# Optimization experiments

Hardware: AMD Instinct MI355X
Metric: run time of the kernel (lower is better)

Reference implementation:

```python
import jax, jax.numpy as jnp
import numpy as np

B, D, T, K = 16, 512, 4096, 1024
COMMIT = 0.25


def setup_inputs() -> dict:
    key = jax.random.key(0)
    kx, ke = jax.random.split(key)
    x = jax.random.normal(kx, (B, D, T), dtype=jnp.float32)
    # nn.init.uniform_(weight, -1/K, 1/K)
    embedding = jax.random.uniform(ke, (K, D), dtype=jnp.float32,
                                   minval=-1.0 / K, maxval=1.0 / K)
    return {"x": x, "embedding": embedding}


def reference(x, embedding):
    # x: [B, D, T] -> [B, T, D]
    xt = jnp.transpose(x, (0, 2, 1))
    xf = xt.reshape(-1, xt.shape[-1])  # [N, D], N = B*T
    dist = (jnp.sum(xf * xf, axis=1, keepdims=True)
            + jnp.sum(embedding * embedding, axis=1)
            - 2.0 * (xf @ embedding.T))
    idx = jnp.argmin(dist, axis=1)  # [N]
    # one-hot @ embedding == gather
    quantized = jnp.take(embedding, idx, axis=0).reshape(xt.shape)  # [B, T, D]
    commitment_loss = COMMIT * jnp.mean((jax.lax.stop_gradient(quantized) - xt) ** 2)
    embedding_loss = jnp.mean((quantized - jax.lax.stop_gradient(xt)) ** 2)
    loss = commitment_loss + embedding_loss
    # straight-through estimator
    quantized_st = xt + jax.lax.stop_gradient(quantized - xt)
    encoding_indices = idx.reshape(xt.shape[0], xt.shape[1], 1)
    return quantized_st, loss, encoding_indices
```

## Files before the change

### kernel.cpp

```cpp
#include <hip/hip_runtime.h>

#define BB 16
#define DD 512
#define TT 4096
#define KK 1024
#define NN (BB*TT)
#define RWS 64
#define BT 1024
#define NW 16
#define MARGIN 1e-3f
#define CM 6
#define PM 384
#define XLD 516
#define NPART (NN/RWS)

typedef __attribute__((ext_vector_type(8))) short short8v;
typedef __attribute__((ext_vector_type(4))) float f32x4;

__device__ __forceinline__ unsigned short f2bf(float f) {
    unsigned int u = __float_as_uint(f);
    unsigned int r = (u + 0x7fffu + ((u >> 16) & 1u)) >> 16;
    return (unsigned short)r;
}

__device__ __forceinline__ float pw128_sq_strided(const float* a, int stride) {
    float V[16];
    #pragma unroll
    for (int l = 0; l < 16; ++l) {
        float q[8];
        #pragma unroll
        for (int k = 0; k < 8; ++k) {
            float e = a[(l + 16 * k) * stride];
            q[k] = __fmul_rn(e, e);
        }
        V[l] = __fadd_rn(__fadd_rn(__fadd_rn(q[0], q[1]), __fadd_rn(q[2], q[3])),
                         __fadd_rn(__fadd_rn(q[4], q[5]), __fadd_rn(q[6], q[7])));
    }
    float u[8];
    #pragma unroll
    for (int l = 0; l < 8; ++l) u[l] = __fadd_rn(V[l], V[l + 8]);
    float v[4];
    #pragma unroll
    for (int l = 0; l < 4; ++l) v[l] = __fadd_rn(u[l], u[l + 4]);
    return __fadd_rn(__fadd_rn(v[0], v[2]), __fadd_rn(v[1], v[3]));
}
__device__ __forceinline__ float pw512_sq_strided(const float* a, int stride) {
    float p0 = pw128_sq_strided(a, stride);
    float p1 = pw128_sq_strided(a + 128 * stride, stride);
    float p2 = pw128_sq_strided(a + 256 * stride, stride);
    float p3 = pw128_sq_strided(a + 384 * stride, stride);
    return __fadd_rn(__fadd_rn(p0, p1), __fadd_rn(p2, p3));
}

__global__ void enorms_exact(const float* __restrict__ E, float* __restrict__ se) {
    int i = blockIdx.x * blockDim.x + threadIdx.x;
    if (i < KK) se[i] = pw512_sq_strided(E + (long)i * DD, 1);
}

__global__ void pack_e(const float* __restrict__ E, unsigned short* __restrict__ Bph) {
    int i = blockIdx.x * blockDim.x + threadIdx.x;
    if (i >= KK * DD / 2) return;
    int c = i >> 8;
    int k = (i & 255) * 2;
    float2 v = *reinterpret_cast<const float2*>(E + ((long)c << 9) + k);
    int lane = (c & 15) + ((k >> 3) & 3) * 16;
    int hw = (((c >> 4) * 16 + (k >> 5)) * 64 + lane) * 8 + (k & 7);
    unsigned int pk = (unsigned int)f2bf(v.x) | ((unsigned int)f2bf(v.y) << 16);
    *reinterpret_cast<unsigned int*>(Bph + hw) = pk;
}

__device__ __forceinline__ short8v build_frag_rm(const float* __restrict__ row, int c0) {
    union { short8v v; unsigned int wd[4]; } u;
    float4 a = *reinterpret_cast<const float4*>(row + c0);
    float4 b = *reinterpret_cast<const float4*>(row + c0 + 4);
    asm("v_cvt_pk_bf16_f32 %0, %1, %2" : "=v"(u.wd[0]) : "v"(a.x), "v"(a.y));
    asm("v_cvt_pk_bf16_f32 %0, %1, %2" : "=v"(u.wd[1]) : "v"(a.z), "v"(a.w));
    asm("v_cvt_pk_bf16_f32 %0, %1, %2" : "=v"(u.wd[2]) : "v"(b.x), "v"(b.y));
    asm("v_cvt_pk_bf16_f32 %0, %1, %2" : "=v"(u.wd[3]) : "v"(b.z), "v"(b.w));
    return u.v;
}

__global__ __launch_bounds__(BT)
void vq_fused(const float* __restrict__ x, const float* __restrict__ E,
              const unsigned short* __restrict__ Bph,
              const float* __restrict__ se,
              double* __restrict__ partials, float* __restrict__ out) {
    __shared__ __align__(16) float xsf[RWS * XLD];
    __shared__ float wrowmin[NW * RWS];
    __shared__ float gthr[RWS];
    __shared__ int   rcnt[RWS];
    __shared__ unsigned short rc[RWS][CM];
    __shared__ int   prow[PM];
    __shared__ int   pcand[PM];
    __shared__ unsigned long long rmin[RWS];
    __shared__ float sxs[RWS];
    __shared__ int   fidx[RWS];
    __shared__ int   oflag[RWS];
    __shared__ double wloss[NW];
    __shared__ int   pcnt, oany;

    const int tid  = threadIdx.x;
    const int w    = tid >> 6;
    const int lane = tid & 63;
    const int blk  = blockIdx.x;
    const int b    = blk >> 6;
    const int t0   = (blk & 63) * RWS;
    const long nbase = (long)b * TT + t0;
    const float* xb = x + (long)b * DD * TT + t0;

    if (tid < RWS) { rcnt[tid] = 0; rmin[tid] = ~0ull; oflag[tid] = 0; fidx[tid] = -1; }
    if (tid == 0) { pcnt = 0; oany = 0; }

    #pragma unroll
    for (int it = 0; it < 8; ++it) {
        int flat = it * BT + tid;
        int d  = flat >> 4;
        int r4 = (flat & 15) * 4;
        float4 v = *reinterpret_cast<const float4*>(xb + (long)d * TT + r4);
        xsf[(r4 + 0) * XLD + d] = v.x;
        xsf[(r4 + 1) * XLD + d] = v.y;
        xsf[(r4 + 2) * XLD + d] = v.z;
        xsf[(r4 + 3) * XLD + d] = v.w;
    }
    __syncthreads();

    f32x4 acc[4][4];
    #pragma unroll
    for (int m = 0; m < 4; ++m)
        #pragma unroll
        for (int n = 0; n < 4; ++n)
            acc[m][n] = (f32x4){0.f, 0.f, 0.f, 0.f};

    const short8v* Bhv = (const short8v*)Bph;
    {
        const int rl  = lane & 15;
        const int lg8 = (lane >> 4) * 8;
        for (int kk = 0; kk < 16; ++kk) {
            short8v bh[4];
            #pragma unroll
            for (int n = 0; n < 4; ++n)
                bh[n] = Bhv[((w * 4 + n) * 16 + kk) * 64 + lane];
            short8v ah[4];
            #pragma unroll
            for (int m = 0; m < 4; ++m)
                ah[m] = build_frag_rm(xsf + (m * 16 + rl) * XLD, kk * 32 + lg8);
            #pragma unroll
            for (int n = 0; n < 4; ++n)
                #pragma unroll
                for (int m = 0; m < 4; ++m)
                    acc[m][n] = __builtin_amdgcn_mfma_f32_16x16x32_bf16(ah[m], bh[n], acc[m][n], 0, 0, 0);
        }
    }

    float sef[4];
    #pragma unroll
    for (int n = 0; n < 4; ++n) sef[n] = se[w * 64 + n * 16 + (lane & 15)];

    #pragma unroll
    for (int m = 0; m < 4; ++m) {
        #pragma unroll
        for (int r4 = 0; r4 < 4; ++r4) {
            float mn = 1e30f;
            #pragma unroll
            for (int n = 0; n < 4; ++n)
                mn = fminf(mn, fmaf(-2.f, acc[m][n][r4], sef[n]));
            #pragma unroll
            for (int off = 1; off < 16; off <<= 1)
                mn = fminf(mn, __shfl_xor(mn, off, 64));
            if ((lane & 15) == 0)
                wrowmin[w * RWS + m * 16 + (lane >> 4) * 4 + r4] = mn;
        }
    }
    __syncthreads();

    if (tid < RWS) {
        float g = 1e30f;
        #pragma unroll
        for (int ww = 0; ww < NW; ++ww)
            g = fminf(g, wrowmin[ww * RWS + tid]);
        gthr[tid] = g + MARGIN;
    }
    __syncthreads();

    #pragma unroll
    for (int m = 0; m < 4; ++m) {
        #pragma unroll
        for (int r4 = 0; r4 < 4; ++r4) {
            int row = m * 16 + (lane >> 4) * 4 + r4;
            float th = gthr[row];
            #pragma unroll
            for (int n = 0; n < 4; ++n) {
                float sc = fmaf(-2.f, acc[m][n][r4], sef[n]);
                if (sc <= th) {
                    int pos = atomicAdd(&rcnt[row], 1);
                    if (pos < CM)
                        rc[row][pos] = (unsigned short)(w * 64 + n * 16 + (lane & 15));
                }
            }
        }
    }
    {
        int r = tid >> 4, l = tid & 15;
        const float* bp = xsf + r * XLD;
        float pblk[4];
        #pragma unroll
        for (int kb = 0; kb < 4; ++kb) {
            float q[8];
            #pragma unroll
            for (int k = 0; k < 8; ++k) {
                float e = bp[kb * 128 + l + 16 * k];
                q[k] = __fmul_rn(e, e);
            }
            float V = __fadd_rn(__fadd_rn(__fadd_rn(q[0], q[1]), __fadd_rn(q[2], q[3])),
                                __fadd_rn(__fadd_rn(q[4], q[5]), __fadd_rn(q[6], q[7])));
            V = __fadd_rn(V, __shfl_xor(V, 8, 16));
            V = __fadd_rn(V, __shfl_xor(V, 4, 16));
            V = __fadd_rn(V, __shfl_xor(V, 2, 16));
            V = __fadd_rn(V, __shfl_xor(V, 1, 16));
            pblk[kb] = V;
        }
        if (l == 0)
            sxs[r] = __fadd_rn(__fadd_rn(pblk[0], pblk[1]), __fadd_rn(pblk[2], pblk[3]));
    }
    __syncthreads();

    if (tid < RWS) {
        int cnt = rcnt[tid];
        if (cnt == 1) {
            fidx[tid] = (int)rc[tid][0];
        } else if (cnt <= CM) {
            int base = atomicAdd(&pcnt, cnt);
            for (int i = 0; i < cnt; ++i) {
                prow[base + i]  = tid;
                pcand[base + i] = (int)rc[tid][i];
            }
        } else {
            oflag[tid] = 1;
            atomicOr(&oany, 1);
        }
    }
    __syncthreads();

    const int np = (pcnt < PM) ? pcnt : PM;
    {
        int p = lane * NW + w;
        if (p < np) {
            int r = prow[p], c = pcand[p];
            const float4* Ep4 = reinterpret_cast<const float4*>(E + (long)c * DD);
            const float4* Xp4 = reinterpret_cast<const float4*>(xsf + r * XLD);
            float g = 0.f;
            #pragma unroll 4
            for (int jj = 0; jj < 128; ++jj) {
                float4 e4 = Ep4[jj], x4 = Xp4[jj];
                g = __fmaf_rn(x4.x, e4.x, g);
                g = __fmaf_rn(x4.y, e4.y, g);
                g = __fmaf_rn(x4.z, e4.z, g);
                g = __fmaf_rn(x4.w, e4.w, g);
            }
            float t1 = __fadd_rn(sxs[r], se[c]);
            float d  = __fsub_rn(t1, __fmul_rn(2.f, g));
            unsigned int bb = __float_as_uint(d);
            unsigned int u  = (bb & 0x80000000u) ? ~bb : (bb | 0x80000000u);
            atomicMin(&rmin[r], ((unsigned long long)u << 10) | (unsigned int)c);
        }
    }
    __syncthreads();

    if (tid < RWS && fidx[tid] < 0 && !oflag[tid])
        fidx[tid] = (int)(rmin[tid] & 0x3ffu);

    if (oany) {
        for (int r = 0; r < RWS; ++r) {
            if (!oflag[r]) continue;
            const float4* Xp4 = reinterpret_cast<const float4*>(xsf + r * XLD);
            int c = tid;
            const float4* Ep4 = reinterpret_cast<const float4*>(E + (long)c * DD);
            float g = 0.f;
            #pragma unroll 4
            for (int jj = 0; jj < 128; ++jj) {
                float4 e4 = Ep4[jj], x4 = Xp4[jj];
                g = __fmaf_rn(x4.x, e4.x, g);
                g = __fmaf_rn(x4.y, e4.y, g);
                g = __fmaf_rn(x4.z, e4.z, g);
                g = __fmaf_rn(x4.w, e4.w, g);
            }
            float bd = __fsub_rn(__fadd_rn(sxs[r], se[c]), __fmul_rn(2.f, g));
            int bi = c;
            #pragma unroll
            for (int off = 32; off; off >>= 1) {
                float tv = __shfl_down(bd, off, 64);
                int   ti = __shfl_down(bi, off, 64);
                if (tv < bd || (tv == bd && ti < bi)) { bd = tv; bi = ti; }
            }
            if (lane == 0) {
                unsigned int bb = __float_as_uint(bd);
                unsigned int u  = (bb & 0x80000000u) ? ~bb : (bb | 0x80000000u);
                atomicMin(&rmin[r], ((unsigned long long)u << 10) | (unsigned int)bi);
            }
            __syncthreads();
            if (tid == 0) fidx[r] = (int)(rmin[r] & 0x3ffu);
        }
    }
    __syncthreads();

    if (tid < RWS)
        out[(size_t)NN * DD + 1 + nbase + tid] = (float)fidx[tid];

    double lacc = 0.0;
    #pragma unroll
    for (int it = 0; it < 8; ++it) {
        int flat = it * BT + tid;
        int r = flat >> 7;
        int j = (flat & 127) * 4;
        int idx = fidx[r];
        float4 ev = *reinterpret_cast<const float4*>(E + (long)idx * DD + j);
        float4 xv = *reinterpret_cast<const float4*>(&xsf[r * XLD + j]);
        float d0 = __fsub_rn(ev.x, xv.x);
        float d1 = __fsub_rn(ev.y, xv.y);
        float d2 = __fsub_rn(ev.z, xv.z);
        float d3 = __fsub_rn(ev.w, xv.w);
        float4 st;
        st.x = __fadd_rn(xv.x, d0); st.y = __fadd_rn(xv.y, d1);
        st.z = __fadd_rn(xv.z, d2); st.w = __fadd_rn(xv.w, d3);
        *reinterpret_cast<float4*>(out + (size_t)(nbase + r) * DD + j) = st;
        lacc += (double)d0 * d0 + (double)d1 * d1 + (double)d2 * d2 + (double)d3 * d3;
    }
    #pragma unroll
    for (int off = 32; off; off >>= 1) lacc += __shfl_down(lacc, off, 64);
    if (lane == 0) wloss[w] = lacc;
    __syncthreads();
    if (tid == 0) {
        double s = 0.0;
        #pragma unroll
        for (int ww = 0; ww < NW; ++ww) s += wloss[ww];
        partials[blk] = s;
    }
}

__global__ void finalize_kernel(const double* __restrict__ partials, float* __restrict__ out) {
    __shared__ double sm[16];
    const int tid = threadIdx.x;
    const int w = tid >> 6, lane = tid & 63;
    double a = partials[tid];
    #pragma unroll
    for (int off = 32; off; off >>= 1) a += __shfl_down(a, off, 64);
    if (lane == 0) sm[w] = a;
    __syncthreads();
    if (tid == 0) {
        double s = 0.0;
        #pragma unroll
        for (int i = 0; i < 16; ++i) s += sm[i];
        out[(size_t)NN * DD] = (float)(1.25 * s / ((double)NN * DD));
    }
}

extern "C" void kernel_launch(void* const* d_in, const int* in_sizes, int n_in,
                              void* d_out, int out_size, void* d_ws, size_t ws_size,
                              hipStream_t stream) {
    const float* x = (const float*)d_in[0];
    const float* E = (const float*)d_in[1];
    float* out = (float*)d_out;
    double* partials = (double*)d_ws;
    float* se = (float*)((char*)d_ws + 32768);
    unsigned short* Bph = (unsigned short*)((char*)d_ws + 65536);

    enorms_exact<<<4, 256, 0, stream>>>(E, se);
    pack_e<<<(KK * DD / 2) / 256, 256, 0, stream>>>(E, Bph);
    vq_fused<<<NPART, BT, 0, stream>>>(x, E, Bph, se, partials, out);
    finalize_kernel<<<1, 1024, 0, stream>>>(partials, out);
}
```

Before: 258.6 us.

## Halve rows per block, widen per-wave codebook tile, rewrite transposed x load

Each block now handles 32 rows with 8 waves of 512 threads instead of 64 rows with 16 waves, and each wave covers 128 codebook entries with a 2x8 MFMA accumulator tile instead of 4x4. The grid doubles, the finalize kernel sums two partials per thread, and the overflow fallback loops over two codes per thread. The x tile load is rewritten so each lane reads 8 strided d values for one row and writes them as contiguous float4 stores into shared memory. The aim is to shrink shared memory per block for better occupancy and to cut LDS bank conflicts in the transpose, at the cost of loading each B fragment once per 32 rows rather than once per 64.

```diff
diff --git a/kernel.cpp b/kernel.cpp
--- a/kernel.cpp
+++ b/kernel.cpp
@@ -5,12 +5,12 @@
 #define TT 4096
 #define KK 1024
 #define NN (BB*TT)
-#define RWS 64
-#define BT 1024
-#define NW 16
+#define RWS 32
+#define BT 512
+#define NW 8
 #define MARGIN 1e-3f
 #define CM 6
-#define PM 384
+#define PM 192
 #define XLD 516
 #define NPART (NN/RWS)
 
@@ -103,32 +103,38 @@
     const int w    = tid >> 6;
     const int lane = tid & 63;
     const int blk  = blockIdx.x;
-    const int b    = blk >> 6;
-    const int t0   = (blk & 63) * RWS;
+    const int b    = blk >> 7;
+    const int t0   = (blk & 127) * RWS;
     const long nbase = (long)b * TT + t0;
     const float* xb = x + (long)b * DD * TT + t0;
 
     if (tid < RWS) { rcnt[tid] = 0; rmin[tid] = ~0ull; oflag[tid] = 0; fidx[tid] = -1; }
     if (tid == 0) { pcnt = 0; oany = 0; }
 
-    #pragma unroll
-    for (int it = 0; it < 8; ++it) {
-        int flat = it * BT + tid;
-        int d  = flat >> 4;
-        int r4 = (flat & 15) * 4;
-        float4 v = *reinterpret_cast<const float4*>(xb + (long)d * TT + r4);
-        xsf[(r4 + 0) * XLD + d] = v.x;
-        xsf[(r4 + 1) * XLD + d] = v.y;
-        xsf[(r4 + 2) * XLD + d] = v.z;
-        xsf[(r4 + 3) * XLD + d] = v.w;
-    }
-    __syncthreads();
-
-    f32x4 acc[4][4];
-    #pragma unroll
-    for (int m = 0; m < 4; ++m)
-        #pragma unroll
-        for (int n = 0; n < 4; ++n)
+    {
+        const int r  = lane & 31;
+        const int dh = lane >> 5;
+        const float* xbl = xb + r;
+        #pragma unroll
+        for (int it = 0; it < 4; ++it) {
+            int d0 = ((it * NW + w) * 2 + dh) * 8;
+            float v[8];
+            #pragma unroll
+            for (int jj = 0; jj < 8; ++jj)
+                v[jj] = xbl[(long)(d0 + jj) * TT];
+            float4 lo = {v[0], v[1], v[2], v[3]};
+            float4 hi = {v[4], v[5], v[6], v[7]};
+            *reinterpret_cast<float4*>(&xsf[r * XLD + d0])     = lo;
+            *reinterpret_cast<float4*>(&xsf[r * XLD + d0 + 4]) = hi;
+        }
+    }
+    __syncthreads();
+
+    f32x4 acc[2][8];
+    #pragma unroll
+    for (int m = 0; m < 2; ++m)
+        #pragma unroll
+        for (int n = 0; n < 8; ++n)
             acc[m][n] = (f32x4){0.f, 0.f, 0.f, 0.f};
 
     const short8v* Bhv = (const short8v*)Bph;
@@ -136,33 +142,37 @@
         const int rl  = lane & 15;
         const int lg8 = (lane >> 4) * 8;
         for (int kk = 0; kk < 16; ++kk) {
-            short8v bh[4];
-            #pragma unroll
-            for (int n = 0; n < 4; ++n)
-                bh[n] = Bhv[((w * 4 + n) * 16 + kk) * 64 + lane];
-            short8v ah[4];
-            #pragma unroll
-            for (int m = 0; m < 4; ++m)
+            short8v ah[2];
+            #pragma unroll
+            for (int m = 0; m < 2; ++m)
                 ah[m] = build_frag_rm(xsf + (m * 16 + rl) * XLD, kk * 32 + lg8);
             #pragma unroll
-            for (int n = 0; n < 4; ++n)
+            for (int nh = 0; nh < 2; ++nh) {
+                short8v bh[4];
                 #pragma unroll
-                for (int m = 0; m < 4; ++m)
-                    acc[m][n] = __builtin_amdgcn_mfma_f32_16x16x32_bf16(ah[m], bh[n], acc[m][n], 0, 0, 0);
-        }
-    }
-
-    float sef[4];
-    #pragma unroll
-    for (int n = 0; n < 4; ++n) sef[n] = se[w * 64 + n * 16 + (lane & 15)];
-
-    #pragma unroll
-    for (int m = 0; m < 4; ++m) {
+                for (int q = 0; q < 4; ++q)
+                    bh[q] = Bhv[((w * 8 + nh * 4 + q) * 16 + kk) * 64 + lane];
+                #pragma unroll
+                for (int q = 0; q < 4; ++q)
+                    #pragma unroll
+                    for (int m = 0; m < 2; ++m)
+                        acc[m][nh * 4 + q] = __builtin_amdgcn_mfma_f32_16x16x32_bf16(
+                            ah[m], bh[q], acc[m][nh * 4 + q], 0, 0, 0);
+            }
+        }
+    }
+
+    float sef[8];
+    #pragma unroll
+    for (int n = 0; n < 8; ++n) sef[n] = se[w * 128 + n * 16 + (lane & 15)];
+
+    #pragma unroll
+    for (int m = 0; m < 2; ++m) {
         #pragma unroll
         for (int r4 = 0; r4 < 4; ++r4) {
             float mn = 1e30f;
             #pragma unroll
-            for (int n = 0; n < 4; ++n)
+            for (int n = 0; n < 8; ++n)
                 mn = fminf(mn, fmaf(-2.f, acc[m][n][r4], sef[n]));
             #pragma unroll
             for (int off = 1; off < 16; off <<= 1)
@@ -183,18 +193,18 @@
     __syncthreads();
 
     #pragma unroll
-    for (int m = 0; m < 4; ++m) {
+    for (int m = 0; m < 2; ++m) {
         #pragma unroll
         for (int r4 = 0; r4 < 4; ++r4) {
             int row = m * 16 + (lane >> 4) * 4 + r4;
             float th = gthr[row];
             #pragma unroll
-            for (int n = 0; n < 4; ++n) {
+            for (int n = 0; n < 8; ++n) {
                 float sc = fmaf(-2.f, acc[m][n][r4], sef[n]);
                 if (sc <= th) {
                     int pos = atomicAdd(&rcnt[row], 1);
                     if (pos < CM)
-                        rc[row][pos] = (unsigned short)(w * 64 + n * 16 + (lane & 15));
+                        rc[row][pos] = (unsigned short)(w * 128 + n * 16 + (lane & 15));
                 }
             }
         }
@@ -273,19 +283,23 @@
         for (int r = 0; r < RWS; ++r) {
             if (!oflag[r]) continue;
             const float4* Xp4 = reinterpret_cast<const float4*>(xsf + r * XLD);
-            int c = tid;
-            const float4* Ep4 = reinterpret_cast<const float4*>(E + (long)c * DD);
-            float g = 0.f;
-            #pragma unroll 4
-            for (int jj = 0; jj < 128; ++jj) {
-                float4 e4 = Ep4[jj], x4 = Xp4[jj];
-                g = __fmaf_rn(x4.x, e4.x, g);
-                g = __fmaf_rn(x4.y, e4.y, g);
-                g = __fmaf_rn(x4.z, e4.z, g);
-                g = __fmaf_rn(x4.w, e4.w, g);
-            }
-            float bd = __fsub_rn(__fadd_rn(sxs[r], se[c]), __fmul_rn(2.f, g));
-            int bi = c;
+            float bd = 1e30f; int bi = KK;
+            #pragma unroll
+            for (int q = 0; q < 2; ++q) {
+                int c = q * BT + tid;
+                const float4* Ep4 = reinterpret_cast<const float4*>(E + (long)c * DD);
+                float g = 0.f;
+                #pragma unroll 4
+                for (int jj = 0; jj < 128; ++jj) {
+                    float4 e4 = Ep4[jj], x4 = Xp4[jj];
+                    g = __fmaf_rn(x4.x, e4.x, g);
+                    g = __fmaf_rn(x4.y, e4.y, g);
+                    g = __fmaf_rn(x4.z, e4.z, g);
+                    g = __fmaf_rn(x4.w, e4.w, g);
+                }
+                float d = __fsub_rn(__fadd_rn(sxs[r], se[c]), __fmul_rn(2.f, g));
+                if (d < bd) { bd = d; bi = c; }
+            }
             #pragma unroll
             for (int off = 32; off; off >>= 1) {
                 float tv = __shfl_down(bd, off, 64);
@@ -341,7 +355,7 @@
     __shared__ double sm[16];
     const int tid = threadIdx.x;
     const int w = tid >> 6, lane = tid & 63;
-    double a = partials[tid];
+    double a = partials[tid] + partials[tid + 1024];
     #pragma unroll
     for (int off = 32; off; off >>= 1) a += __shfl_down(a, off, 64);
     if (lane == 0) sm[w] = a;
```

Result: faster. 224.5 us (-13.2%).
